# Kernel optimization log

Hardware: AMD Instinct MI355X
Metric: run time of the kernel (lower is better)

## Reference

```python
import jax, jax.numpy as jnp
import numpy as np


def _rope_tables(seq_len, head_dim):
    # freqs: [seq_len, head_dim//2]
    inv = 1.0 / (10000.0 ** (jnp.arange(0, head_dim, 2, dtype=jnp.float32) / head_dim))
    pos = jnp.arange(seq_len, dtype=jnp.float32)
    f = jnp.outer(pos, inv)
    return jnp.cos(f), jnp.sin(f)


def _apply_rope(x, cos, sin):
    # x: [B, H, T, D]; interleaved pairs (even, odd) rotated
    x1 = x[..., 0::2]
    x2 = x[..., 1::2]
    r1 = x1 * cos - x2 * sin
    r2 = x1 * sin + x2 * cos
    return jnp.stack([r1, r2], axis=-1).reshape(x.shape)


def setup_inputs() -> dict:
    key = jax.random.key(0)
    k1, k2, k3, k4 = jax.random.split(key, 4)
    B, T, C = 2, 2048, 2048
    s = 1.0 / np.sqrt(C)
    return {
        "x": jax.random.normal(k1, (B, T, C), dtype=jnp.float32),
        "W_qk": jax.random.normal(k2, (C, 2 * C), dtype=jnp.float32) * s,
        "W_v": jax.random.normal(k3, (C, C), dtype=jnp.float32) * s,
        "W_o": jax.random.normal(k4, (C, C), dtype=jnp.float32) * s,
        "n_heads": 16,
    }


def reference(x, W_qk, W_v, W_o, n_heads):
    B, T, C = x.shape
    H = n_heads
    D = C // H
    qk = x @ W_qk                      # [B, T, 2C]
    q, k = jnp.split(qk, 2, axis=-1)
    v = x @ W_v
    q = q.reshape(B, T, H, D).transpose(0, 2, 1, 3)  # [B,H,T,D]
    k = k.reshape(B, T, H, D).transpose(0, 2, 1, 3)
    v = v.reshape(B, T, H, D).transpose(0, 2, 1, 3)
    cos, sin = _rope_tables(T, D)      # [T, D//2]
    q = _apply_rope(q, cos, sin)
    k = _apply_rope(k, cos, sin)
    scores = jnp.einsum("bhqd,bhkd->bhqk", q, k) / jnp.sqrt(jnp.float32(D))
    attn = jax.nn.softmax(scores, axis=-1)
    out = jnp.einsum("bhqk,bhkd->bhqd", attn, v)
    out = out.transpose(0, 2, 1, 3).reshape(B, T, C)
    return out @ W_o, k, v
```

## Files before the change

### kernel.cpp

```cpp
#include <hip/hip_runtime.h>
#include <cstdint>

typedef __bf16 bf16x8 __attribute__((ext_vector_type(8)));
typedef float  f32x4  __attribute__((ext_vector_type(4)));
typedef float  f32x16 __attribute__((ext_vector_type(16)));
typedef unsigned short u16;
typedef unsigned int   u32;

static __device__ __forceinline__ u16 f2bf(float f) {
    u32 u = __float_as_uint(f);
    u += 0x7FFFu + ((u >> 16) & 1u);
    return (u16)(u >> 16);
}

static __device__ __forceinline__ void glds16(const u16* src, u16* dst) {
    __builtin_amdgcn_global_load_lds((const __attribute__((address_space(1))) void*)src,
                                     (__attribute__((address_space(3))) void*)dst, 16, 0, 0);
}

__global__ void k_cvt(const float* __restrict__ in, u16* __restrict__ out, int n4) {
    int i = blockIdx.x * 256 + threadIdx.x;
    if (i >= n4) return;
    float4 v = ((const float4*)in)[i];
    uint2 o;
    o.x = f2bf(v.x) | ((u32)f2bf(v.y) << 16);
    o.y = f2bf(v.z) | ((u32)f2bf(v.w) << 16);
    ((uint2*)out)[i] = o;
}

__global__ void k_transp(const float* __restrict__ W, u16* __restrict__ Wt, int K, int N) {
    __shared__ float tile[32][33];
    int tx = threadIdx.x & 31, ty = threadIdx.x >> 5;
    int k0 = blockIdx.y * 32, n0 = blockIdx.x * 32;
#pragma unroll
    for (int j = 0; j < 4; ++j)
        tile[ty + j * 8][tx] = W[(size_t)(k0 + ty + j * 8) * N + n0 + tx];
    __syncthreads();
#pragma unroll
    for (int j = 0; j < 4; ++j)
        Wt[(size_t)(n0 + ty + j * 8) * K + k0 + tx] = f2bf(tile[tx][ty + j * 8]);
}

__global__ void k_tables(float* __restrict__ cosT, float* __restrict__ sinT) {
    int i = blockIdx.x * 256 + threadIdx.x;
    int t = i >> 6, d = i & 63;
    double inv = pow(10000.0, -(double)d / 64.0);
    double f = (double)t * inv;
    cosT[i] = (float)cos(f);
    sinT[i] = (float)sin(f);
}

template <int EPI>
__global__ __launch_bounds__(256, 2)
void k_gemm(const u16* __restrict__ A, const u16* __restrict__ Bt,
            float* __restrict__ C, u16* __restrict__ C2,
            int M, int N, int K) {
    __shared__ u16 Al[128 * 32];
    __shared__ u16 Bl[128 * 32];
    const int tid = threadIdx.x;
    const int wv = tid >> 6, ln = tid & 63;
    const int wm = wv >> 1, wn = wv & 1;
    const int lr = ln & 15, lk = ln >> 4;
    const int bm = blockIdx.y, bn = blockIdx.x;
    const u16* Ab = A + (size_t)bm * 128 * K;
    const u16* Bb = Bt + (size_t)bn * 128 * K;
    f32x4 acc[4][4] = {};
    const int c0 = wv * 128 + ln, c1 = c0 + 64;
    const int r0 = c0 >> 2, g0 = c0 & 3, r1 = c1 >> 2, g1 = c1 & 3;
    for (int kt = 0; kt < (K >> 5); ++kt) {
        __syncthreads();
        glds16(Ab + (size_t)r0 * K + kt * 32 + g0 * 8, Al + (wv * 2) * 512);
        glds16(Ab + (size_t)r1 * K + kt * 32 + g1 * 8, Al + (wv * 2 + 1) * 512);
        glds16(Bb + (size_t)r0 * K + kt * 32 + g0 * 8, Bl + (wv * 2) * 512);
        glds16(Bb + (size_t)r1 * K + kt * 32 + g1 * 8, Bl + (wv * 2 + 1) * 512);
        __syncthreads();
        bf16x8 af[4], bfr[4];
#pragma unroll
        for (int m = 0; m < 4; ++m)
            af[m] = *(const bf16x8*)(Al + (wm * 64 + m * 16 + lr) * 32 + lk * 8);
#pragma unroll
        for (int n = 0; n < 4; ++n)
            bfr[n] = *(const bf16x8*)(Bl + (wn * 64 + n * 16 + lr) * 32 + lk * 8);
#pragma unroll
        for (int m = 0; m < 4; ++m)
#pragma unroll
            for (int n = 0; n < 4; ++n)
                acc[m][n] = __builtin_amdgcn_mfma_f32_16x16x32_bf16(af[m], bfr[n], acc[m][n], 0, 0, 0);
    }
    const int gr_base = bm * 128 + wm * 64;
    const int gc_base = bn * 128 + wn * 64;
    if (EPI == 0) {
#pragma unroll
        for (int m = 0; m < 4; ++m) {
            int gr0 = gr_base + m * 16 + lk * 4;
#pragma unroll
            for (int n = 0; n < 4; ++n) {
                int gc = gc_base + n * 16 + lr;
#pragma unroll
                for (int r = 0; r < 4; ++r)
                    C[(size_t)(gr0 + r) * N + gc] = acc[m][n][r];
            }
        }
    } else {
#pragma unroll
        for (int m = 0; m < 4; ++m) {
            int gr0 = gr_base + m * 16 + lk * 4;
            int b_ = gr0 >> 11, t0 = gr0 & 2047;
#pragma unroll
            for (int n = 0; n < 4; ++n) {
                int gc = gc_base + n * 16 + lr;
                int h_ = gc >> 7, d_ = gc & 127;
                float v0 = acc[m][n][0], v1 = acc[m][n][1], v2 = acc[m][n][2], v3 = acc[m][n][3];
                float* vo = C + ((size_t)(b_ * 16 + h_) * 2048 + t0) * 128 + d_;
                vo[0] = v0; vo[128] = v1; vo[256] = v2; vo[384] = v3;
                uint2 pk;
                pk.x = f2bf(v0) | ((u32)f2bf(v1) << 16);
                pk.y = f2bf(v2) | ((u32)f2bf(v3) << 16);
                *(uint2*)(C2 + ((size_t)(b_ * 16 + h_) * 128 + d_) * 2048 + t0) = pk;
            }
        }
    }
}

__global__ void k_rope(const float* __restrict__ qk, const float* __restrict__ cosT,
                       const float* __restrict__ sinT, u16* __restrict__ qb,
                       u16* __restrict__ kb, float* __restrict__ kout) {
    int i = blockIdx.x * 256 + threadIdx.x;
    int p = i & 63;
    int h = (i >> 6) & 15;
    int t = (i >> 10) & 2047;
    int b = i >> 21;
    const float* row = qk + (size_t)((b << 11) + t) * 4096;
    float c = cosT[(t << 6) + p], s = sinT[(t << 6) + p];
    size_t o = ((size_t)((b * 16 + h) * 2048 + t) << 7) + 2 * p;
    float2 q2 = *(const float2*)(row + h * 128 + 2 * p);
    float r1 = q2.x * c - q2.y * s;
    float r2 = q2.x * s + q2.y * c;
    *(u32*)(qb + o) = f2bf(r1) | ((u32)f2bf(r2) << 16);
    float2 k2 = *(const float2*)(row + 2048 + h * 128 + 2 * p);
    r1 = k2.x * c - k2.y * s;
    r2 = k2.x * s + k2.y * c;
    *(u32*)(kb + o) = f2bf(r1) | ((u32)f2bf(r2) << 16);
    *(float2*)(kout + o) = make_float2(r1, r2);
}

__global__ __launch_bounds__(256, 2)
void k_attn(const u16* __restrict__ qb, const u16* __restrict__ kb,
            const u16* __restrict__ vbt, u16* __restrict__ aout) {
    __shared__ u16 Kl[64 * 128];
    __shared__ u16 Vl[128 * 64];
    __shared__ u16 Pl[4 * 32 * 64];
    __shared__ float scl[4 * 32];
    const int tid = threadIdx.x;
    const int wv = tid >> 6, ln = tid & 63;
    const int lq = ln & 31, hi = ln >> 5;
    const int qt = blockIdx.x, h = blockIdx.y, b = blockIdx.z;
    const size_t bh = (size_t)(b * 16 + h);
    const u16* qbase = qb + bh * 2048 * 128;
    const u16* kbase = kb + bh * 2048 * 128;
    const u16* vbase = vbt + bh * 128 * 2048;
    const int q0 = qt * 128 + wv * 32;
    bf16x8 qf[8];
    {
        const u16* qrow = qbase + (size_t)(q0 + lq) * 128;
#pragma unroll
        for (int t = 0; t < 8; ++t)
            qf[t] = *(const bf16x8*)(qrow + t * 16 + hi * 8);
    }
    f32x16 O[4] = {};
    float m_run = -3.0e38f, l_run = 0.0f;
    const float SCL2 = 0.12751637469644085f;
    const int swz = (lq & 7) << 4;
    const char* KlB = (const char*)Kl;
    const char* VlB = (const char*)Vl;
    char* PlB = (char*)Pl + wv * 4096 + lq * 128;

    for (int kt = 0; kt < 32; ++kt) {
        __syncthreads();
#pragma unroll
        for (int i = 0; i < 4; ++i) {
            int c = (wv * 4 + i) * 64 + ln;
            int key = c >> 4, g = c & 15;
            glds16(kbase + (size_t)(kt * 64 + key) * 128 + (g ^ (key & 7)) * 8,
                   Kl + (wv * 4 + i) * 512);
        }
#pragma unroll
        for (int i = 0; i < 4; ++i) {
            int c = (wv * 4 + i) * 64 + ln;
            int dd = c >> 3, g = c & 7;
            glds16(vbase + (size_t)dd * 2048 + kt * 64 + (g ^ (dd & 7)) * 8,
                   Vl + (wv * 4 + i) * 512);
        }
        __syncthreads();
        f32x16 s0 = {}, s1 = {};
#pragma unroll
        for (int t = 0; t < 8; ++t) {
            int off = (t * 32 + hi * 16) ^ swz;
            bf16x8 k0 = *(const bf16x8*)(KlB + lq * 256 + off);
            bf16x8 k1 = *(const bf16x8*)(KlB + (32 + lq) * 256 + off);
            s0 = __builtin_amdgcn_mfma_f32_32x32x16_bf16(k0, qf[t], s0, 0, 0, 0);
            s1 = __builtin_amdgcn_mfma_f32_32x32x16_bf16(k1, qf[t], s1, 0, 0, 0);
        }
        float mt = fmaxf(s0[0], s1[0]);
#pragma unroll
        for (int r = 1; r < 16; ++r) mt = fmaxf(mt, fmaxf(s0[r], s1[r]));
        mt = fmaxf(mt, __shfl_xor(mt, 32));
        float m_new = fmaxf(m_run, mt);
        float alpha = exp2f((m_run - m_new) * SCL2);
        f32x16 p0, p1;
        float lt = 0.0f;
#pragma unroll
        for (int r = 0; r < 16; ++r) {
            p0[r] = exp2f((s0[r] - m_new) * SCL2);
            p1[r] = exp2f((s1[r] - m_new) * SCL2);
            lt += p0[r] + p1[r];
        }
        lt += __shfl_xor(lt, 32);
        l_run = l_run * alpha + lt;
        if (__any(mt > m_run)) {
            if (hi == 0) scl[wv * 32 + lq] = alpha;
            asm volatile("s_waitcnt lgkmcnt(0)" ::: "memory");
#pragma unroll
            for (int t2 = 0; t2 < 4; ++t2) {
                f32x4 a4 = *(const f32x4*)(scl + wv * 32 + t2 * 8 + hi * 4);
#pragma unroll
                for (int n = 0; n < 4; ++n)
#pragma unroll
                    for (int j = 0; j < 4; ++j)
                        O[n][t2 * 4 + j] *= a4[j];
            }
        }
        m_run = m_new;
#pragma unroll
        for (int t2 = 0; t2 < 4; ++t2) {
            uint2 w0, w1;
            w0.x = f2bf(p0[t2 * 4 + 0]) | ((u32)f2bf(p0[t2 * 4 + 1]) << 16);
            w0.y = f2bf(p0[t2 * 4 + 2]) | ((u32)f2bf(p0[t2 * 4 + 3]) << 16);
            w1.x = f2bf(p1[t2 * 4 + 0]) | ((u32)f2bf(p1[t2 * 4 + 1]) << 16);
            w1.y = f2bf(p1[t2 * 4 + 2]) | ((u32)f2bf(p1[t2 * 4 + 3]) << 16);
            *(uint2*)(PlB + ((t2 * 16 + hi * 8) ^ swz)) = w0;
            *(uint2*)(PlB + ((64 + t2 * 16 + hi * 8) ^ swz)) = w1;
        }
        asm volatile("s_waitcnt lgkmcnt(0)" ::: "memory");
#pragma unroll
        for (int t = 0; t < 4; ++t) {
            int koff = t * 32 + hi * 16;
            bf16x8 pa = *(const bf16x8*)(PlB + (koff ^ swz));
#pragma unroll
            for (int n = 0; n < 4; ++n) {
                bf16x8 vb = *(const bf16x8*)(VlB + (n * 32 + lq) * 128 + (koff ^ swz));
                O[n] = __builtin_amdgcn_mfma_f32_32x32x16_bf16(pa, vb, O[n], 0, 0, 0);
            }
        }
    }
    float invl = 1.0f / l_run;
    if (hi == 0) scl[wv * 32 + lq] = invl;
    asm volatile("s_waitcnt lgkmcnt(0)" ::: "memory");
#pragma unroll
    for (int t2 = 0; t2 < 4; ++t2) {
        f32x4 iv = *(const f32x4*)(scl + wv * 32 + t2 * 8 + hi * 4);
#pragma unroll
        for (int j = 0; j < 4; ++j) {
            int row = q0 + t2 * 8 + hi * 4 + j;
            u16* orow = aout + (size_t)(b * 2048 + row) * 2048 + h * 128;
#pragma unroll
            for (int n = 0; n < 4; ++n)
                orow[n * 32 + lq] = f2bf(O[n][t2 * 4 + j] * iv[j]);
        }
    }
}

extern "C" void kernel_launch(void* const* d_in, const int* in_sizes, int n_in,
                              void* d_out, int out_size, void* d_ws, size_t ws_size,
                              hipStream_t stream) {
    const float* x   = (const float*)d_in[0];
    const float* Wqk = (const float*)d_in[1];
    const float* Wv  = (const float*)d_in[2];
    const float* Wo  = (const float*)d_in[3];
    float* out0 = (float*)d_out;
    float* kout = out0 + 8388608;
    float* vout = out0 + 16777216;
    char* ws = (char*)d_ws;
    const size_t MB = 1024 * 1024;
    u16*   xb   = (u16*)(ws);
    u16*   wqkT = (u16*)(ws + 16 * MB);
    u16*   wvT  = (u16*)(ws + 32 * MB);
    u16*   woT  = (u16*)(ws + 40 * MB);
    float* cosT = (float*)(ws + 48 * MB);
    float* sinT = (float*)(ws + 48 * MB + 512 * 1024);
    u16*   qbf  = (u16*)(ws + 49 * MB);
    u16*   kbf  = (u16*)(ws + 65 * MB);
    float* qkf  = (float*)(ws + 81 * MB);
    u16*   vbt  = (u16*)(ws + 81 * MB);
    u16*   abf  = (u16*)(ws + 97 * MB);

    k_cvt<<<8192, 256, 0, stream>>>(x, xb, 2097152);
    k_transp<<<dim3(128, 64), 256, 0, stream>>>(Wqk, wqkT, 2048, 4096);
    k_transp<<<dim3(64, 64), 256, 0, stream>>>(Wv, wvT, 2048, 2048);
    k_transp<<<dim3(64, 64), 256, 0, stream>>>(Wo, woT, 2048, 2048);
    k_tables<<<512, 256, 0, stream>>>(cosT, sinT);
    k_gemm<0><<<dim3(32, 32), 256, 0, stream>>>(xb, wqkT, qkf, nullptr, 4096, 4096, 2048);
    k_rope<<<16384, 256, 0, stream>>>(qkf, cosT, sinT, qbf, kbf, kout);
    k_gemm<1><<<dim3(16, 32), 256, 0, stream>>>(xb, wvT, vout, vbt, 4096, 2048, 2048);
    k_attn<<<dim3(16, 16, 2), 256, 0, stream>>>(qbf, kbf, vbt, abf);
    k_gemm<0><<<dim3(16, 32), 256, 0, stream>>>(abf, woT, out0, nullptr, 4096, 2048, 2048);
}
```

Baseline: 489.8 us.

## Double-buffer K/V tiles, keep P in registers, lazy softmax rescale

Double-buffers the K and V shared-memory tiles so the next tile's global-to-LDS load is issued while the current tile is computed, leaving one barrier per iteration. The P tile no longer makes a round trip through shared memory; it is rearranged between lane halves with cross-lane shuffles into the MFMA operand layout. The running max is only updated, and O rescaled, when the new max exceeds the old one by more than a threshold, which skips most rescales but lets exponentials grow up to 2^8 before renormalisation. Packing to bf16 now uses the native conversion. The cost is twice the K/V LDS footprint and a small numeric-range risk from the deferred max update.

New measurement: 475.7 us. 1.03x faster.

```diff
diff --git a/kernel.cpp b/kernel.cpp
--- a/kernel.cpp
+++ b/kernel.cpp
@@ -2,15 +2,22 @@
 #include <cstdint>
 
 typedef __bf16 bf16x8 __attribute__((ext_vector_type(8)));
+typedef __bf16 bf16x2 __attribute__((ext_vector_type(2)));
 typedef float  f32x4  __attribute__((ext_vector_type(4)));
 typedef float  f32x16 __attribute__((ext_vector_type(16)));
+typedef unsigned int u32;
+typedef u32 u32x4 __attribute__((ext_vector_type(4)));
 typedef unsigned short u16;
-typedef unsigned int   u32;
 
 static __device__ __forceinline__ u16 f2bf(float f) {
     u32 u = __float_as_uint(f);
     u += 0x7FFFu + ((u >> 16) & 1u);
     return (u16)(u >> 16);
+}
+
+static __device__ __forceinline__ u32 pkbf(float a, float b) {
+    bf16x2 v; v[0] = (__bf16)a; v[1] = (__bf16)b;
+    return __builtin_bit_cast(u32, v);
 }
 
 static __device__ __forceinline__ void glds16(const u16* src, u16* dst) {
@@ -147,9 +154,8 @@
 __global__ __launch_bounds__(256, 2)
 void k_attn(const u16* __restrict__ qb, const u16* __restrict__ kb,
             const u16* __restrict__ vbt, u16* __restrict__ aout) {
-    __shared__ u16 Kl[64 * 128];
-    __shared__ u16 Vl[128 * 64];
-    __shared__ u16 Pl[4 * 32 * 64];
+    __shared__ u16 Kl[2][64 * 128];
+    __shared__ u16 Vl[2][128 * 64];
     __shared__ float scl[4 * 32];
     const int tid = threadIdx.x;
     const int wv = tid >> 6, ln = tid & 63;
@@ -171,27 +177,32 @@
     float m_run = -3.0e38f, l_run = 0.0f;
     const float SCL2 = 0.12751637469644085f;
     const int swz = (lq & 7) << 4;
-    const char* KlB = (const char*)Kl;
-    const char* VlB = (const char*)Vl;
-    char* PlB = (char*)Pl + wv * 4096 + lq * 128;
-
-    for (int kt = 0; kt < 32; ++kt) {
-        __syncthreads();
+
+    auto STAGE = [&](int buf, int kt) {
 #pragma unroll
         for (int i = 0; i < 4; ++i) {
             int c = (wv * 4 + i) * 64 + ln;
             int key = c >> 4, g = c & 15;
             glds16(kbase + (size_t)(kt * 64 + key) * 128 + (g ^ (key & 7)) * 8,
-                   Kl + (wv * 4 + i) * 512);
+                   Kl[buf] + (wv * 4 + i) * 512);
         }
 #pragma unroll
         for (int i = 0; i < 4; ++i) {
             int c = (wv * 4 + i) * 64 + ln;
             int dd = c >> 3, g = c & 7;
             glds16(vbase + (size_t)dd * 2048 + kt * 64 + (g ^ (dd & 7)) * 8,
-                   Vl + (wv * 4 + i) * 512);
-        }
-        __syncthreads();
+                   Vl[buf] + (wv * 4 + i) * 512);
+        }
+    };
+
+    STAGE(0, 0);
+    __syncthreads();
+
+    for (int kt = 0; kt < 32; ++kt) {
+        const int cur = kt & 1;
+        if (kt < 31) STAGE(cur ^ 1, kt + 1);
+        const char* KlB = (const char*)Kl[cur];
+        const char* VlB = (const char*)Vl[cur];
         f32x16 s0 = {}, s1 = {};
 #pragma unroll
         for (int t = 0; t < 8; ++t) {
@@ -205,19 +216,9 @@
 #pragma unroll
         for (int r = 1; r < 16; ++r) mt = fmaxf(mt, fmaxf(s0[r], s1[r]));
         mt = fmaxf(mt, __shfl_xor(mt, 32));
-        float m_new = fmaxf(m_run, mt);
-        float alpha = exp2f((m_run - m_new) * SCL2);
-        f32x16 p0, p1;
-        float lt = 0.0f;
-#pragma unroll
-        for (int r = 0; r < 16; ++r) {
-            p0[r] = exp2f((s0[r] - m_new) * SCL2);
-            p1[r] = exp2f((s1[r] - m_new) * SCL2);
-            lt += p0[r] + p1[r];
-        }
-        lt += __shfl_xor(lt, 32);
-        l_run = l_run * alpha + lt;
-        if (__any(mt > m_run)) {
+        if (__any((mt - m_run) * SCL2 > 8.0f)) {
+            float m_new = fmaxf(m_run, mt);
+            float alpha = exp2f((m_run - m_new) * SCL2);
             if (hi == 0) scl[wv * 32 + lq] = alpha;
             asm volatile("s_waitcnt lgkmcnt(0)" ::: "memory");
 #pragma unroll
@@ -229,29 +230,49 @@
                     for (int j = 0; j < 4; ++j)
                         O[n][t2 * 4 + j] *= a4[j];
             }
-        }
-        m_run = m_new;
-#pragma unroll
-        for (int t2 = 0; t2 < 4; ++t2) {
-            uint2 w0, w1;
-            w0.x = f2bf(p0[t2 * 4 + 0]) | ((u32)f2bf(p0[t2 * 4 + 1]) << 16);
-            w0.y = f2bf(p0[t2 * 4 + 2]) | ((u32)f2bf(p0[t2 * 4 + 3]) << 16);
-            w1.x = f2bf(p1[t2 * 4 + 0]) | ((u32)f2bf(p1[t2 * 4 + 1]) << 16);
-            w1.y = f2bf(p1[t2 * 4 + 2]) | ((u32)f2bf(p1[t2 * 4 + 3]) << 16);
-            *(uint2*)(PlB + ((t2 * 16 + hi * 8) ^ swz)) = w0;
-            *(uint2*)(PlB + ((64 + t2 * 16 + hi * 8) ^ swz)) = w1;
-        }
-        asm volatile("s_waitcnt lgkmcnt(0)" ::: "memory");
+            l_run *= alpha;
+            m_run = m_new;
+        }
+        f32x16 p0, p1;
+        float lt = 0.0f;
+#pragma unroll
+        for (int r = 0; r < 16; ++r) {
+            p0[r] = exp2f((s0[r] - m_run) * SCL2);
+            p1[r] = exp2f((s1[r] - m_run) * SCL2);
+            lt += p0[r] + p1[r];
+        }
+        lt += __shfl_xor(lt, 32);
+        l_run += lt;
+        u32 ua[8], ub[8];
+#pragma unroll
+        for (int a = 0; a < 4; ++a) {
+            ua[a]     = pkbf(p0[4 * a + 0], p0[4 * a + 1]);
+            ub[a]     = pkbf(p0[4 * a + 2], p0[4 * a + 3]);
+            ua[4 + a] = pkbf(p1[4 * a + 0], p1[4 * a + 1]);
+            ub[4 + a] = pkbf(p1[4 * a + 2], p1[4 * a + 3]);
+        }
 #pragma unroll
         for (int t = 0; t < 4; ++t) {
-            int koff = t * 32 + hi * 16;
-            bf16x8 pa = *(const bf16x8*)(PlB + (koff ^ swz));
+            u32 v0 = hi ? ua[2 * t] : ua[2 * t + 1];
+            u32 v1 = hi ? ub[2 * t] : ub[2 * t + 1];
+            u32 x0 = (u32)__shfl_xor((int)v0, 32);
+            u32 x1 = (u32)__shfl_xor((int)v1, 32);
+            u32 o0 = hi ? ua[2 * t + 1] : ua[2 * t];
+            u32 o1 = hi ? ub[2 * t + 1] : ub[2 * t];
+            u32x4 ww;
+            ww.x = hi ? x0 : o0;
+            ww.y = hi ? x1 : o1;
+            ww.z = hi ? o0 : x0;
+            ww.w = hi ? o1 : x1;
+            bf16x8 pa = __builtin_bit_cast(bf16x8, ww);
+            int koff = (t * 32 + hi * 16);
 #pragma unroll
             for (int n = 0; n < 4; ++n) {
                 bf16x8 vb = *(const bf16x8*)(VlB + (n * 32 + lq) * 128 + (koff ^ swz));
                 O[n] = __builtin_amdgcn_mfma_f32_32x32x16_bf16(pa, vb, O[n], 0, 0, 0);
             }
         }
+        __syncthreads();
     }
     float invl = 1.0f / l_run;
     if (hi == 0) scl[wv * 32 + lq] = invl;
```
